# Kernel optimization log

Hardware: AMD Instinct MI355X
Metric: run time of the kernel (lower is better)

The kernel has to match this reference:

```python
import jax, jax.numpy as jnp
import numpy as np

HIDDEN = 1024
N_HEADS = 16
HEAD_DIM = HIDDEN // N_HEADS


def setup_inputs() -> dict:
    key = jax.random.key(0)
    ks = jax.random.split(key, 10)
    s = 0.02
    return {
        "x": jax.random.normal(ks[0], (2, 2048, HIDDEN), dtype=jnp.float32),
        "wq_w": jax.random.normal(ks[1], (HEAD_DIM, HEAD_DIM), dtype=jnp.float32) * s,
        "wq_b": jax.random.normal(ks[2], (HEAD_DIM,), dtype=jnp.float32) * s,
        "wk_w": jax.random.normal(ks[3], (HEAD_DIM, HEAD_DIM), dtype=jnp.float32) * s,
        "wk_b": jax.random.normal(ks[4], (HEAD_DIM,), dtype=jnp.float32) * s,
        "wv_w": jax.random.normal(ks[5], (HEAD_DIM, HEAD_DIM), dtype=jnp.float32) * s,
        "wv_b": jax.random.normal(ks[6], (HEAD_DIM,), dtype=jnp.float32) * s,
        "wo_w": jax.random.normal(ks[7], (HIDDEN, HIDDEN), dtype=jnp.float32) * s,
        "wo_b": jax.random.normal(ks[8], (HIDDEN,), dtype=jnp.float32) * s,
    }


def reference(x, wq_w, wq_b, wk_w, wk_b, wv_w, wv_b, wo_w, wo_b):
    B, S, _ = x.shape
    # Faithful to torch: plain reshape (view), NOT a transpose-based head split.
    xh = x.reshape(B, N_HEADS, S, HEAD_DIM)  # [B,H,S,D]
    # torch Linear: y = x @ W.T + b
    Q = jnp.einsum('bhsd,ed->bhse', xh, wq_w) + wq_b
    K = jnp.einsum('bhsd,ed->bhse', xh, wk_w) + wk_b
    V = jnp.einsum('bhsd,ed->bhse', xh, wv_w) + wv_b
    scale = 1.0 / jnp.sqrt(jnp.float32(HEAD_DIM))
    scores = jnp.einsum('bhqd,bhkd->bhqk', Q, K) * scale  # [B,H,S,S]
    attn = jax.nn.softmax(scores, axis=-1)
    ctx = jnp.einsum('bhqk,bhkd->bhqd', attn, V)  # [B,H,S,D]
    out = ctx.reshape(B, S, HIDDEN)
    return out @ wo_w.T + wo_b
```

## Files before the change

kernel.cpp:

```cpp
#include <hip/hip_runtime.h>
#include <hip/hip_bf16.h>

#define SEQ 2048
#define BHCOUNT 32
#define NROWS (BHCOUNT*SEQ)

typedef unsigned short u16;
typedef unsigned int u32;
using bf16x8 = __attribute__((ext_vector_type(8))) short;
using f32x4  = __attribute__((ext_vector_type(4))) float;

__device__ __forceinline__ float bf2f(u16 h) {
    return __uint_as_float(((u32)h) << 16);
}
__device__ __forceinline__ u16 f2bf(float f) {
    u32 u = __float_as_uint(f);
    u32 r = (u + 0x7FFFu + ((u >> 16) & 1u)) >> 16;
    return (u16)r;
}
__device__ __forceinline__ float fexp2(float x) {
    float r; asm("v_exp_f32 %0, %1" : "=v"(r) : "v"(x)); return r;
}

__device__ __forceinline__ void gload16(const u16* g, u16* l) {
    __builtin_amdgcn_global_load_lds(
        (const __attribute__((address_space(1))) u32*)g,
        (__attribute__((address_space(3))) u32*)l, 16, 0, 0);
}

__device__ __forceinline__ void cvt8(const float* src, float sc, u16* o) {
    float4 a = *(const float4*)src;
    float4 b = *(const float4*)(src + 4);
    o[0]=f2bf(a.x*sc); o[1]=f2bf(a.y*sc); o[2]=f2bf(a.z*sc); o[3]=f2bf(a.w*sc);
    o[4]=f2bf(b.x*sc); o[5]=f2bf(b.y*sc); o[6]=f2bf(b.z*sc); o[7]=f2bf(b.w*sc);
}

__global__ __launch_bounds__(256) void qkv_wconv_kernel(
    const float* __restrict__ x,
    const float* __restrict__ wq, const float* __restrict__ bq,
    const float* __restrict__ wk, const float* __restrict__ bk,
    const float* __restrict__ wv, const float* __restrict__ bv,
    const float* __restrict__ wo,
    u16* __restrict__ Q, u16* __restrict__ K, u16* __restrict__ Vg,
    u16* __restrict__ wob_t)
{
    __shared__ u16 xs[128*64];
    __shared__ u16 ws[192*64];
    __shared__ float bs[192];
    const int t = threadIdx.x;

    if (blockIdx.x >= 512) {
        int g = (blockIdx.x - 512)*256 + t;
        int tile = g >> 9, within = g & 511;
        int row = within >> 3, ks = within & 7;
        int cb = tile >> 4, kt = tile & 15;
        u16 o[8];
        cvt8(&wo[(size_t)(cb*64 + row)*1024 + kt*64 + ks*8], 1.f, o);
        *(uint4*)&wob_t[(size_t)g*8] = *(uint4*)o;
        return;
    }

    const int wid = t >> 6, lane = t & 63;
    const int ln = lane & 15, g4 = lane >> 4;
    const int blk = blockIdx.x;
    const int m0 = blk * 128;
    const int bh = blk >> 4;
    const int ktg0 = (blk & 15) * 2;
    const float qscale = 0.125f * 1.44269504f;

    #pragma unroll
    for (int c = 0; c < 6; ++c) {
        int slot = c*256 + t;
        int row = slot >> 3, ks = slot & 7;
        const float* wsrc = (c < 2) ? wq : (c < 4) ? wk : wv;
        float sc = (c < 2) ? qscale : 1.f;
        u16 o[8];
        cvt8(&wsrc[(row & 63)*64 + ks*8], sc, o);
        *(uint4*)&ws[row*64 + ((ks ^ (row & 7)) << 3)] = *(uint4*)o;
    }
    #pragma unroll
    for (int c = 0; c < 4; ++c) {
        int slot = c*256 + t;
        int row = slot >> 3, ks = slot & 7;
        u16 o[8];
        cvt8(&x[(size_t)(m0 + row)*64 + ks*8], 1.f, o);
        *(uint4*)&xs[row*64 + ((ks ^ (row & 7)) << 3)] = *(uint4*)o;
    }
    if (t < 192) {
        int p = t >> 6, e = t & 63;
        bs[t] = (p == 0) ? bq[e]*qscale : (p == 1) ? bk[e] : bv[e];
    }
    __syncthreads();

    bf16x8 af[2][2];
    #pragma unroll
    for (int mf = 0; mf < 2; ++mf)
        #pragma unroll
        for (int kf = 0; kf < 2; ++kf) {
            int arow = wid*32 + mf*16 + ln;
            af[mf][kf] = *(const bf16x8*)&xs[arow*64 + (((kf*4 + g4) ^ (arow & 7)) << 3)];
        }

    #pragma unroll
    for (int p = 0; p < 2; ++p) {
        bf16x8 bfr[4][2];
        #pragma unroll
        for (int nt = 0; nt < 4; ++nt)
            #pragma unroll
            for (int kf = 0; kf < 2; ++kf) {
                int brow = p*64 + nt*16 + ln;
                bfr[nt][kf] = *(const bf16x8*)&ws[brow*64 + (((kf*4 + g4) ^ (ln & 7)) << 3)];
            }
        f32x4 acc[2][4];
        #pragma unroll
        for (int mf = 0; mf < 2; ++mf)
            #pragma unroll
            for (int nt = 0; nt < 4; ++nt) acc[mf][nt] = (f32x4){0.f,0.f,0.f,0.f};
        #pragma unroll
        for (int kf = 0; kf < 2; ++kf)
            #pragma unroll
            for (int mf = 0; mf < 2; ++mf)
                #pragma unroll
                for (int nt = 0; nt < 4; ++nt)
                    acc[mf][nt] = __builtin_amdgcn_mfma_f32_16x16x32_bf16(
                        af[mf][kf], bfr[nt][kf], acc[mf][nt], 0, 0, 0);
        u16* dst = p ? K : Q;
        #pragma unroll
        for (int mf = 0; mf < 2; ++mf)
            #pragma unroll
            for (int nt = 0; nt < 4; ++nt) {
                float bv4 = bs[p*64 + nt*16 + ln];
                #pragma unroll
                for (int r = 0; r < 4; ++r)
                    dst[(size_t)(m0 + wid*32 + mf*16 + g4*4 + r)*64 + nt*16 + ln]
                        = f2bf(acc[mf][nt][r] + bv4);
            }
    }

    bf16x8 wvf[4][2];
    #pragma unroll
    for (int et = 0; et < 4; ++et)
        #pragma unroll
        for (int kf = 0; kf < 2; ++kf) {
            int brow = 128 + et*16 + ln;
            wvf[et][kf] = *(const bf16x8*)&ws[brow*64 + (((kf*4 + g4) ^ (ln & 7)) << 3)];
        }
    f32x4 vacc[4][2];
    #pragma unroll
    for (int et = 0; et < 4; ++et)
        #pragma unroll
        for (int st = 0; st < 2; ++st) vacc[et][st] = (f32x4){0.f,0.f,0.f,0.f};
    #pragma unroll
    for (int kf = 0; kf < 2; ++kf)
        #pragma unroll
        for (int et = 0; et < 4; ++et)
            #pragma unroll
            for (int st = 0; st < 2; ++st)
                vacc[et][st] = __builtin_amdgcn_mfma_f32_16x16x32_bf16(
                    wvf[et][kf], af[st][kf], vacc[et][st], 0, 0, 0);

    __syncthreads();
    u16* vstage = xs;
    #pragma unroll
    for (int et = 0; et < 4; ++et)
        #pragma unroll
        for (int st = 0; st < 2; ++st)
            #pragma unroll
            for (int r = 0; r < 4; ++r) {
                int e = et*16 + g4*4 + r;
                int s = wid*32 + st*16 + ln;
                vstage[e*128 + ((s + 2*e) & 127)] = f2bf(vacc[et][st][r] + bs[128 + e]);
            }
    __syncthreads();

    #pragma unroll
    for (int c = 0; c < 8; ++c) {
        int j = c*256 + t;
        int kt2 = j >> 10, within = j & 1023;
        int ee = within >> 4, kp0 = (within & 15) * 4;
        int sbase = ((kp0 & 4) << 3) | ((kp0 & 32) >> 1) | ((kp0 & 24) >> 1);
        u16 o[4];
        #pragma unroll
        for (int i = 0; i < 4; ++i)
            o[i] = vstage[ee*128 + ((kt2*64 + sbase + i + 2*ee) & 127)];
        *(uint2*)&Vg[((size_t)bh*32 + ktg0 + kt2)*4096 + ee*64 + kp0] = *(uint2*)o;
    }
}

__global__ __launch_bounds__(256, 2) void attn_kernel(
    const u16* __restrict__ Q, const u16* __restrict__ K,
    const u16* __restrict__ Vg, u16* __restrict__ ctx)
{
    __shared__ u16 Kls[2][4096];
    __shared__ u16 Vls[2][4096];

    const int t = threadIdx.x;
    const int wid = t >> 6, lane = t & 63;
    const int ln = lane & 15, g4 = lane >> 4;
    const int bh = blockIdx.y;
    const size_t base   = (size_t)bh * SEQ * 64;
    const size_t vgbase = (size_t)bh * 32 * 4096;
    const int q0 = blockIdx.x * 128 + wid * 32;

    int goff[2];
    #pragma unroll
    for (int c = 0; c < 2; ++c) {
        int s = c*256 + t;
        int row = s >> 3, ks = s & 7;
        goff[c] = row*64 + ((ks ^ (row & 7)) << 3);
    }

    int foff[4][2];
    #pragma unroll
    for (int nt = 0; nt < 4; ++nt)
        #pragma unroll
        for (int kf = 0; kf < 2; ++kf) {
            int frow = nt*16 + ln;
            foff[nt][kf] = frow*64 + (((kf*4 + g4) ^ (frow & 7)) << 3);
        }

    bf16x8 qf0[2], qf1[2];
    #pragma unroll
    for (int kf = 0; kf < 2; ++kf) {
        qf0[kf] = *(const bf16x8*)&Q[base + (size_t)(q0 + ln)*64      + kf*32 + g4*8];
        qf1[kf] = *(const bf16x8*)&Q[base + (size_t)(q0 + 16 + ln)*64 + kf*32 + g4*8];
    }

    bf16x8 ones;
    #pragma unroll
    for (int i = 0; i < 8; ++i) ones[i] = (short)0x3F80;

    f32x4 oacc0[4], oacc1[4];
    #pragma unroll
    for (int i = 0; i < 4; ++i) {
        oacc0[i] = (f32x4){0.f, 0.f, 0.f, 0.f};
        oacc1[i] = (f32x4){0.f, 0.f, 0.f, 0.f};
    }
    f32x4 lacc0 = (f32x4){0.f, 0.f, 0.f, 0.f};
    f32x4 lacc1 = (f32x4){0.f, 0.f, 0.f, 0.f};

    #pragma unroll
    for (int c = 0; c < 2; ++c) {
        gload16(&K [base   + goff[c]], &Kls[0][c*2048 + wid*512]);
        gload16(&Vg[vgbase + goff[c]], &Vls[0][c*2048 + wid*512]);
    }
    __syncthreads();

    for (int kt2 = 0; kt2 < 16; ++kt2) {
        #pragma unroll
        for (int half = 0; half < 2; ++half) {
            const int kt = kt2*2 + half;
            if (kt < 31) {
                #pragma unroll
                for (int c = 0; c < 2; ++c) {
                    gload16(&K [base   + (size_t)(kt+1)*4096 + goff[c]],
                            &Kls[half^1][c*2048 + wid*512]);
                    gload16(&Vg[vgbase + (size_t)(kt+1)*4096 + goff[c]],
                            &Vls[half^1][c*2048 + wid*512]);
                }
            }
            const u16* Ks  = Kls[half];
            const u16* Vts = Vls[half];

            f32x4 s0[4], s1[4];
            #pragma unroll
            for (int nt = 0; nt < 4; ++nt) {
                s0[nt] = (f32x4){0.f, 0.f, 0.f, 0.f};
                s1[nt] = (f32x4){0.f, 0.f, 0.f, 0.f};
            }
            __builtin_amdgcn_s_setprio(1);
            #pragma unroll
            for (int nt = 0; nt < 4; ++nt)
                #pragma unroll
                for (int kf = 0; kf < 2; ++kf) {
                    bf16x8 kfr = *(const bf16x8*)&Ks[foff[nt][kf]];
                    s0[nt] = __builtin_amdgcn_mfma_f32_16x16x32_bf16(kfr, qf0[kf], s0[nt], 0, 0, 0);
                    s1[nt] = __builtin_amdgcn_mfma_f32_16x16x32_bf16(kfr, qf1[kf], s1[nt], 0, 0, 0);
                }
            __builtin_amdgcn_s_setprio(0);

            #pragma unroll
            for (int nt = 0; nt < 4; ++nt)
                #pragma unroll
                for (int r = 0; r < 4; ++r) {
                    s0[nt][r] = fexp2(s0[nt][r]);
                    s1[nt][r] = fexp2(s1[nt][r]);
                }

            union PU { u32 w[4]; bf16x8 v; } a0, a1, b0, b1;
            asm("v_cvt_pk_bf16_f32 %0, %1, %2" : "=v"(a0.w[0]) : "v"(s0[0][0]), "v"(s0[0][1]));
            asm("v_cvt_pk_bf16_f32 %0, %1, %2" : "=v"(a0.w[1]) : "v"(s0[0][2]), "v"(s0[0][3]));
            asm("v_cvt_pk_bf16_f32 %0, %1, %2" : "=v"(a0.w[2]) : "v"(s0[2][0]), "v"(s0[2][1]));
            asm("v_cvt_pk_bf16_f32 %0, %1, %2" : "=v"(a0.w[3]) : "v"(s0[2][2]), "v"(s0[2][3]));
            asm("v_cvt_pk_bf16_f32 %0, %1, %2" : "=v"(a1.w[0]) : "v"(s0[1][0]), "v"(s0[1][1]));
            asm("v_cvt_pk_bf16_f32 %0, %1, %2" : "=v"(a1.w[1]) : "v"(s0[1][2]), "v"(s0[1][3]));
            asm("v_cvt_pk_bf16_f32 %0, %1, %2" : "=v"(a1.w[2]) : "v"(s0[3][0]), "v"(s0[3][1]));
            asm("v_cvt_pk_bf16_f32 %0, %1, %2" : "=v"(a1.w[3]) : "v"(s0[3][2]), "v"(s0[3][3]));
            asm("v_cvt_pk_bf16_f32 %0, %1, %2" : "=v"(b0.w[0]) : "v"(s1[0][0]), "v"(s1[0][1]));
            asm("v_cvt_pk_bf16_f32 %0, %1, %2" : "=v"(b0.w[1]) : "v"(s1[0][2]), "v"(s1[0][3]));
            asm("v_cvt_pk_bf16_f32 %0, %1, %2" : "=v"(b0.w[2]) : "v"(s1[2][0]), "v"(s1[2][1]));
            asm("v_cvt_pk_bf16_f32 %0, %1, %2" : "=v"(b0.w[3]) : "v"(s1[2][2]), "v"(s1[2][3]));
            asm("v_cvt_pk_bf16_f32 %0, %1, %2" : "=v"(b1.w[0]) : "v"(s1[1][0]), "v"(s1[1][1]));
            asm("v_cvt_pk_bf16_f32 %0, %1, %2" : "=v"(b1.w[1]) : "v"(s1[1][2]), "v"(s1[1][3]));
            asm("v_cvt_pk_bf16_f32 %0, %1, %2" : "=v"(b1.w[2]) : "v"(s1[3][0]), "v"(s1[3][1]));
            asm("v_cvt_pk_bf16_f32 %0, %1, %2" : "=v"(b1.w[3]) : "v"(s1[3][2]), "v"(s1[3][3]));
            bf16x8 pf0[2] = { a0.v, a1.v };
            bf16x8 pf1[2] = { b0.v, b1.v };

            __builtin_amdgcn_s_setprio(1);
            #pragma unroll
            for (int dt = 0; dt < 4; ++dt)
                #pragma unroll
                for (int kf = 0; kf < 2; ++kf) {
                    bf16x8 vfr = *(const bf16x8*)&Vts[foff[dt][kf]];
                    oacc0[dt] = __builtin_amdgcn_mfma_f32_16x16x32_bf16(pf0[kf], vfr, oacc0[dt], 0, 0, 0);
                    oacc1[dt] = __builtin_amdgcn_mfma_f32_16x16x32_bf16(pf1[kf], vfr, oacc1[dt], 0, 0, 0);
                }
            #pragma unroll
            for (int kf = 0; kf < 2; ++kf) {
                lacc0 = __builtin_amdgcn_mfma_f32_16x16x32_bf16(pf0[kf], ones, lacc0, 0, 0, 0);
                lacc1 = __builtin_amdgcn_mfma_f32_16x16x32_bf16(pf1[kf], ones, lacc1, 0, 0, 0);
            }
            __builtin_amdgcn_s_setprio(0);

            __syncthreads();
        }
    }

    #pragma unroll
    for (int r = 0; r < 4; ++r) {
        float inv0 = 1.f / lacc0[r];
        float inv1 = 1.f / lacc1[r];
        size_t row0 = base + (size_t)(q0 + g4*4 + r)*64;
        size_t row1 = base + (size_t)(q0 + 16 + g4*4 + r)*64;
        #pragma unroll
        for (int dt = 0; dt < 4; ++dt) {
            ctx[row0 + dt*16 + ln] = f2bf(oacc0[dt][r] * inv0);
            ctx[row1 + dt*16 + ln] = f2bf(oacc1[dt][r] * inv1);
        }
    }
}

__global__ __launch_bounds__(256) void oproj_kernel(
    const u16* __restrict__ ctx, const u16* __restrict__ wob_t,
    const float* __restrict__ bo, float* __restrict__ out)
{
    __shared__ u16 Als[2][128*64];
    __shared__ u16 Bls[2][64*64];
    const int t = threadIdx.x;
    const int wid = t >> 6, lane = t & 63;
    const int ln = lane & 15, g4 = lane >> 4;
    const int wr = wid >> 1, wc = wid & 1;
    const int rb = blockIdx.x, cb = blockIdx.y;
    const int m0 = rb * 128;

    int gA[4], gB[2];
    #pragma unroll
    for (int c = 0; c < 4; ++c) {
        int slot = c*256 + t;
        int row = slot >> 3, ks = slot & 7;
        gA[c] = row*1024 + ((ks ^ (row & 7)) << 3);
    }
    #pragma unroll
    for (int c = 0; c < 2; ++c) {
        int slot = c*256 + t;
        int row = slot >> 3, ks = slot & 7;
        gB[c] = row*64 + ((ks ^ (row & 7)) << 3);
    }
    const u16* actx = ctx + (size_t)m0*1024;
    const u16* bw   = wob_t + (size_t)cb*16*4096;

    f32x4 acc[4][2];
    #pragma unroll
    for (int mf = 0; mf < 4; ++mf)
        #pragma unroll
        for (int nf = 0; nf < 2; ++nf)
            acc[mf][nf] = (f32x4){0.f, 0.f, 0.f, 0.f};

    #pragma unroll
    for (int c = 0; c < 4; ++c) gload16(&actx[gA[c]], &Als[0][(c*256+t)*8]);
    #pragma unroll
    for (int c = 0; c < 2; ++c) gload16(&bw[gB[c]],   &Bls[0][(c*256+t)*8]);
    __syncthreads();

    for (int kt2 = 0; kt2 < 8; ++kt2) {
        #pragma unroll
        for (int half = 0; half < 2; ++half) {
            const int kt = kt2*2 + half;
            if (kt < 15) {
                #pragma unroll
                for (int c = 0; c < 4; ++c)
                    gload16(&actx[(kt+1)*64 + gA[c]], &Als[half^1][(c*256+t)*8]);
                #pragma unroll
                for (int c = 0; c < 2; ++c)
                    gload16(&bw[(kt+1)*4096 + gB[c]], &Bls[half^1][(c*256+t)*8]);
            }
            const u16* As = Als[half];
            const u16* Bs = Bls[half];

            __builtin_amdgcn_s_setprio(1);
            #pragma unroll
            for (int kf = 0; kf < 2; ++kf) {
                bf16x8 af[4], bfr[2];
                #pragma unroll
                for (int mf = 0; mf < 4; ++mf) {
                    int arow = wr*64 + mf*16 + ln;
                    af[mf] = *(const bf16x8*)&As[arow*64 + (((kf*4 + g4) ^ (arow & 7)) << 3)];
                }
                #pragma unroll
                for (int nf = 0; nf < 2; ++nf) {
                    int brow = wc*32 + nf*16 + ln;
                    bfr[nf] = *(const bf16x8*)&Bs[brow*64 + (((kf*4 + g4) ^ (brow & 7)) << 3)];
                }
                #pragma unroll
                for (int mf = 0; mf < 4; ++mf)
                    #pragma unroll
                    for (int nf = 0; nf < 2; ++nf)
                        acc[mf][nf] = __builtin_amdgcn_mfma_f32_16x16x32_bf16(
                            af[mf], bfr[nf], acc[mf][nf], 0, 0, 0);
            }
            __builtin_amdgcn_s_setprio(0);

            __syncthreads();
        }
    }

    #pragma unroll
    for (int mf = 0; mf < 4; ++mf)
        #pragma unroll
        for (int r = 0; r < 4; ++r) {
            int m = m0 + wr*64 + mf*16 + g4*4 + r;
            #pragma unroll
            for (int nf = 0; nf < 2; ++nf) {
                int col = cb*64 + wc*32 + nf*16 + ln;
                out[(size_t)m*1024 + col] = acc[mf][nf][r] + bo[col];
            }
        }
}

extern "C" void kernel_launch(void* const* d_in, const int* in_sizes, int n_in,
                              void* d_out, int out_size, void* d_ws, size_t ws_size,
                              hipStream_t stream) {
    (void)in_sizes; (void)n_in; (void)out_size; (void)ws_size;
    const float* x  = (const float*)d_in[0];
    const float* wq = (const float*)d_in[1];
    const float* bq = (const float*)d_in[2];
    const float* wk = (const float*)d_in[3];
    const float* bk = (const float*)d_in[4];
    const float* wv = (const float*)d_in[5];
    const float* bv = (const float*)d_in[6];
    const float* wo = (const float*)d_in[7];
    const float* bo = (const float*)d_in[8];
    float* out = (float*)d_out;

    u16* Qb  = (u16*)d_ws;
    u16* Kb  = Qb + (size_t)NROWS*64;
    u16* Vgb = Kb + (size_t)NROWS*64;
    u16* ctx = Vgb + (size_t)NROWS*64;
    u16* wob_t = ctx + (size_t)NROWS*64;

    qkv_wconv_kernel<<<dim3(1024), 256, 0, stream>>>(
        x, wq, bq, wk, bk, wv, bv, wo, Qb, Kb, Vgb, wob_t);
    attn_kernel<<<dim3(16, 32), 256, 0, stream>>>(Qb, Kb, Vgb, ctx);
    oproj_kernel<<<dim3(32, 16), 256, 0, stream>>>(ctx, wob_t, bo, out);
}
```

Before: 70.76 us.

## Split attention key range across two warp groups and merge partials through LDS

The attention block grows to 512 threads, split into two groups of four warps. Each group handles half of the key tiles with its own double-buffered K/V shared memory. At the end, the second group writes its partial output and row-sum accumulators to LDS and the first group adds them before normalising and storing. This doubles the waves in flight and halves each wave's serial key loop, to hide latency on a grid that was too small to fill the device. In exchange it adds a cross-group LDS reduction, and `__launch_bounds__(512, 4)` caps registers tightly, which may cause spills.

After: 70.10 us. Within noise of the previous version (-0.9%).

```diff
diff --git a/kernel.cpp b/kernel.cpp
--- a/kernel.cpp
+++ b/kernel.cpp
@@ -187,25 +187,29 @@
     }
 }
 
-__global__ __launch_bounds__(256, 2) void attn_kernel(
+__global__ __launch_bounds__(512, 4) void attn_kernel(
     const u16* __restrict__ Q, const u16* __restrict__ K,
     const u16* __restrict__ Vg, u16* __restrict__ ctx)
 {
-    __shared__ u16 Kls[2][4096];
-    __shared__ u16 Vls[2][4096];
+    __shared__ u16 Kls[2][2][4096];
+    __shared__ u16 Vls[2][2][4096];
 
     const int t = threadIdx.x;
     const int wid = t >> 6, lane = t & 63;
+    const int hk = wid >> 2;
+    const int w4 = wid & 3;
+    const int tt = t & 255;
     const int ln = lane & 15, g4 = lane >> 4;
     const int bh = blockIdx.y;
     const size_t base   = (size_t)bh * SEQ * 64;
     const size_t vgbase = (size_t)bh * 32 * 4096;
-    const int q0 = blockIdx.x * 128 + wid * 32;
+    const int q0 = blockIdx.x * 128 + w4 * 32;
+    const int kt0 = hk * 16;
 
     int goff[2];
     #pragma unroll
     for (int c = 0; c < 2; ++c) {
-        int s = c*256 + t;
+        int s = c*256 + tt;
         int row = s >> 3, ks = s & 7;
         goff[c] = row*64 + ((ks ^ (row & 7)) << 3);
     }
@@ -241,26 +245,26 @@
 
     #pragma unroll
     for (int c = 0; c < 2; ++c) {
-        gload16(&K [base   + goff[c]], &Kls[0][c*2048 + wid*512]);
-        gload16(&Vg[vgbase + goff[c]], &Vls[0][c*2048 + wid*512]);
-    }
-    __syncthreads();
-
-    for (int kt2 = 0; kt2 < 16; ++kt2) {
-        #pragma unroll
-        for (int half = 0; half < 2; ++half) {
-            const int kt = kt2*2 + half;
-            if (kt < 31) {
+        gload16(&K [base   + (size_t)kt0*4096 + goff[c]], &Kls[hk][0][c*2048 + w4*512]);
+        gload16(&Vg[vgbase + (size_t)kt0*4096 + goff[c]], &Vls[hk][0][c*2048 + w4*512]);
+    }
+    __syncthreads();
+
+    for (int kt2 = 0; kt2 < 8; ++kt2) {
+        #pragma unroll
+        for (int pb = 0; pb < 2; ++pb) {
+            const int kt = kt2*2 + pb;
+            if (kt < 15) {
                 #pragma unroll
                 for (int c = 0; c < 2; ++c) {
-                    gload16(&K [base   + (size_t)(kt+1)*4096 + goff[c]],
-                            &Kls[half^1][c*2048 + wid*512]);
-                    gload16(&Vg[vgbase + (size_t)(kt+1)*4096 + goff[c]],
-                            &Vls[half^1][c*2048 + wid*512]);
-                }
-            }
-            const u16* Ks  = Kls[half];
-            const u16* Vts = Vls[half];
+                    gload16(&K [base   + (size_t)(kt0+kt+1)*4096 + goff[c]],
+                            &Kls[hk][pb^1][c*2048 + w4*512]);
+                    gload16(&Vg[vgbase + (size_t)(kt0+kt+1)*4096 + goff[c]],
+                            &Vls[hk][pb^1][c*2048 + w4*512]);
+                }
+            }
+            const u16* Ks  = Kls[hk][pb];
+            const u16* Vts = Vls[hk][pb];
 
             f32x4 s0[4], s1[4];
             #pragma unroll
@@ -327,16 +331,38 @@
         }
     }
 
-    #pragma unroll
-    for (int r = 0; r < 4; ++r) {
-        float inv0 = 1.f / lacc0[r];
-        float inv1 = 1.f / lacc1[r];
-        size_t row0 = base + (size_t)(q0 + g4*4 + r)*64;
-        size_t row1 = base + (size_t)(q0 + 16 + g4*4 + r)*64;
+    float* mO = (float*)(&Kls[0][0][0]);
+    float* mL = (float*)(&Vls[0][0][0]);
+    if (hk == 1) {
         #pragma unroll
         for (int dt = 0; dt < 4; ++dt) {
-            ctx[row0 + dt*16 + ln] = f2bf(oacc0[dt][r] * inv0);
-            ctx[row1 + dt*16 + ln] = f2bf(oacc1[dt][r] * inv1);
+            *(f32x4*)&mO[(((w4*2 + 0)*4 + dt)*64 + lane)*4] = oacc0[dt];
+            *(f32x4*)&mO[(((w4*2 + 1)*4 + dt)*64 + lane)*4] = oacc1[dt];
+        }
+        *(f32x4*)&mL[((w4*2 + 0)*64 + lane)*4] = lacc0;
+        *(f32x4*)&mL[((w4*2 + 1)*64 + lane)*4] = lacc1;
+    }
+    __syncthreads();
+    if (hk == 0) {
+        #pragma unroll
+        for (int dt = 0; dt < 4; ++dt) {
+            oacc0[dt] += *(const f32x4*)&mO[(((w4*2 + 0)*4 + dt)*64 + lane)*4];
+            oacc1[dt] += *(const f32x4*)&mO[(((w4*2 + 1)*4 + dt)*64 + lane)*4];
+        }
+        lacc0 += *(const f32x4*)&mL[((w4*2 + 0)*64 + lane)*4];
+        lacc1 += *(const f32x4*)&mL[((w4*2 + 1)*64 + lane)*4];
+
+        #pragma unroll
+        for (int r = 0; r < 4; ++r) {
+            float inv0 = 1.f / lacc0[r];
+            float inv1 = 1.f / lacc1[r];
+            size_t row0 = base + (size_t)(q0 + g4*4 + r)*64;
+            size_t row1 = base + (size_t)(q0 + 16 + g4*4 + r)*64;
+            #pragma unroll
+            for (int dt = 0; dt < 4; ++dt) {
+                ctx[row0 + dt*16 + ln] = f2bf(oacc0[dt][r] * inv0);
+                ctx[row1 + dt*16 + ln] = f2bf(oacc1[dt][r] * inv1);
+            }
         }
     }
 }
@@ -461,6 +487,6 @@
 
     qkv_wconv_kernel<<<dim3(1024), 256, 0, stream>>>(
         x, wq, bq, wk, bk, wv, bv, wo, Qb, Kb, Vgb, wob_t);
-    attn_kernel<<<dim3(16, 32), 256, 0, stream>>>(Qb, Kb, Vgb, ctx);
+    attn_kernel<<<dim3(16, 32), 512, 0, stream>>>(Qb, Kb, Vgb, ctx);
     oproj_kernel<<<dim3(32, 16), 256, 0, stream>>>(ctx, wob_t, bo, out);
 }
```
